# Kernel tuning notes

Measured on AMD Instinct MI355X. Metric: run time of the kernel, lower is better.

The kernel has to match this reference:

```python
import jax, jax.numpy as jnp
import numpy as np

N = 16384   # must equal C**2 so the rel-pos embed broadcasts with x
C = 128     # in_channels
K = 9       # k (min legal for C=128: (2k-1)^2 >= 2C-1)
C_OUT = 256


def setup_inputs() -> dict:
    key = jax.random.key(0)
    k1, k2, k3 = jax.random.split(key, 3)
    x = jax.random.normal(k1, (N, C), dtype=jnp.float32)
    rel_pos_table = jax.random.normal(k2, ((2 * K - 1) ** 2, C), dtype=jnp.float32) * 0.02
    W = jax.random.normal(k3, (2 * C, C_OUT), dtype=jnp.float32) / np.float32(np.sqrt(2 * C))
    b = jnp.zeros((C_OUT,), dtype=jnp.float32)
    return {"x": x, "rel_pos_table": rel_pos_table, "W": W, "b": b}


def _knn_indices(x, k):
    # brute-force kNN (torch_cluster knn_graph, loop=False), dilation=1 -> no edge subsampling
    sq = jnp.sum(x * x, axis=-1)                       # [N]
    d = sq[:, None] + sq[None, :] - 2.0 * (x @ x.T)    # [N, N] squared distances
    d = d.at[jnp.diag_indices(x.shape[0])].set(jnp.inf)  # exclude self-loops
    _, idx = jax.lax.top_k(-d, k)                      # [N, k] nearest neighbors
    return idx


def reference(x, rel_pos_table, W, b):
    n, c = x.shape
    # 1) graph built on RAW x (before rel-pos add), as in the torch forward
    nbr = _knn_indices(x, K)                           # [N, K]
    # 2) learnable relative positional embedding: grid_size = x.shape[1] = C
    ar = jnp.arange(c)
    rel = (ar[:, None] - ar[None, :] + c - 1).reshape(-1)  # [C*C] == [N]
    x = x + rel_pos_table[rel]                         # [N, C]
    # 3) MRConv: max-relative aggregation + concat + 1x1 linear
    x_j = x[nbr]                                       # [N, K, C] neighbor gather
    m = jnp.max(x_j - x[:, None, :], axis=1)           # [N, C] max over neighbors
    return jnp.concatenate([x, m], axis=-1) @ W + b    # [N, C_OUT]
```

## Files before the change

### kernel.cpp

```cpp
#include <hip/hip_runtime.h>

#define NPTS 16384
#define CH 128
#define KNN 9
#define NCAND 12
#define NHALF 4
#define COUT 256
#define RG 16
#define RCAND 3

typedef __attribute__((ext_vector_type(8))) short bf16x8;
typedef __attribute__((ext_vector_type(4))) float f32x4;
typedef __attribute__((address_space(1))) const unsigned gu32;
typedef __attribute__((address_space(3))) unsigned lu32;


__device__ __forceinline__ unsigned bfhi2(float x0, float x1) {
    unsigned u0 = __float_as_uint(x0), u1 = __float_as_uint(x1);
    unsigned r0 = (u0 + 0x7fffu + ((u0 >> 16) & 1u));
    unsigned r1 = (u1 + 0x7fffu + ((u1 >> 16) & 1u));
    return (r0 >> 16) | (r1 & 0xffff0000u);
}

struct TopL {
    float l0,l1,l2,l3,l4,l5,l6,l7,l8,l9,la,lb;
    int   m0,m1,m2,m3,m4,m5,m6,m7,m8,m9,ma,mb;
};
struct Top9 {
    float l0,l1,l2,l3,l4,l5,l6,l7,l8;
    int   m0,m1,m2,m3,m4,m5,m6,m7,m8;
};

__device__ __forceinline__ bool lexlt(float d, int g, float L, int M) {
    return d < L || (d == L && g < M);
}

__device__ __forceinline__ void ins12(TopL& T, float d, int g) {
    if (!lexlt(d, g, T.lb, T.mb)) return;
    bool b0 = lexlt(d,g,T.l0,T.m0);
    bool b1 = lexlt(d,g,T.l1,T.m1);
    bool b2 = lexlt(d,g,T.l2,T.m2);
    bool b3 = lexlt(d,g,T.l3,T.m3);
    bool b4 = lexlt(d,g,T.l4,T.m4);
    bool b5 = lexlt(d,g,T.l5,T.m5);
    bool b6 = lexlt(d,g,T.l6,T.m6);
    bool b7 = lexlt(d,g,T.l7,T.m7);
    bool b8 = lexlt(d,g,T.l8,T.m8);
    bool b9 = lexlt(d,g,T.l9,T.m9);
    bool ba = lexlt(d,g,T.la,T.ma);
    T.lb = ba ? T.la : d;               T.mb = ba ? T.ma : g;
    T.la = b9 ? T.l9 : (ba ? d : T.la); T.ma = b9 ? T.m9 : (ba ? g : T.ma);
    T.l9 = b8 ? T.l8 : (b9 ? d : T.l9); T.m9 = b8 ? T.m8 : (b9 ? g : T.m9);
    T.l8 = b7 ? T.l7 : (b8 ? d : T.l8); T.m8 = b7 ? T.m7 : (b8 ? g : T.m8);
    T.l7 = b6 ? T.l6 : (b7 ? d : T.l7); T.m7 = b6 ? T.m6 : (b7 ? g : T.m7);
    T.l6 = b5 ? T.l5 : (b6 ? d : T.l6); T.m6 = b5 ? T.m5 : (b6 ? g : T.m6);
    T.l5 = b4 ? T.l4 : (b5 ? d : T.l5); T.m5 = b4 ? T.m4 : (b5 ? g : T.m5);
    T.l4 = b3 ? T.l3 : (b4 ? d : T.l4); T.m4 = b3 ? T.m3 : (b4 ? g : T.m4);
    T.l3 = b2 ? T.l2 : (b3 ? d : T.l3); T.m3 = b2 ? T.m2 : (b3 ? g : T.m3);
    T.l2 = b1 ? T.l1 : (b2 ? d : T.l2); T.m2 = b1 ? T.m1 : (b2 ? g : T.m2);
    T.l1 = b0 ? T.l0 : (b1 ? d : T.l1); T.m1 = b0 ? T.m0 : (b1 ? g : T.m1);
    T.l0 = b0 ? d : T.l0;               T.m0 = b0 ? g : T.m0;
}

__device__ __forceinline__ void ins9(Top9& T, float d, int g) {
    if (!lexlt(d, g, T.l8, T.m8)) return;
    bool b0 = lexlt(d,g,T.l0,T.m0);
    bool b1 = lexlt(d,g,T.l1,T.m1);
    bool b2 = lexlt(d,g,T.l2,T.m2);
    bool b3 = lexlt(d,g,T.l3,T.m3);
    bool b4 = lexlt(d,g,T.l4,T.m4);
    bool b5 = lexlt(d,g,T.l5,T.m5);
    bool b6 = lexlt(d,g,T.l6,T.m6);
    bool b7 = lexlt(d,g,T.l7,T.m7);
    T.l8 = b7 ? T.l7 : d;               T.m8 = b7 ? T.m7 : g;
    T.l7 = b6 ? T.l6 : (b7 ? d : T.l7); T.m7 = b6 ? T.m6 : (b7 ? g : T.m7);
    T.l6 = b5 ? T.l5 : (b6 ? d : T.l6); T.m6 = b5 ? T.m5 : (b6 ? g : T.m6);
    T.l5 = b4 ? T.l4 : (b5 ? d : T.l5); T.m5 = b4 ? T.m4 : (b5 ? g : T.m5);
    T.l4 = b3 ? T.l3 : (b4 ? d : T.l4); T.m4 = b3 ? T.m3 : (b4 ? g : T.m4);
    T.l3 = b2 ? T.l2 : (b3 ? d : T.l3); T.m3 = b2 ? T.m2 : (b3 ? g : T.m3);
    T.l2 = b1 ? T.l1 : (b2 ? d : T.l2); T.m2 = b1 ? T.m1 : (b2 ? g : T.m2);
    T.l1 = b0 ? T.l0 : (b1 ? d : T.l1); T.m1 = b0 ? T.m0 : (b1 ? g : T.m1);
    T.l0 = b0 ? d : T.l0;               T.m0 = b0 ? g : T.m0;
}

__device__ __forceinline__ void merge_shfl(TopL& T, int mask) {
    TopL o;
    o.l0=__shfl_xor(T.l0,mask); o.m0=__shfl_xor(T.m0,mask);
    o.l1=__shfl_xor(T.l1,mask); o.m1=__shfl_xor(T.m1,mask);
    o.l2=__shfl_xor(T.l2,mask); o.m2=__shfl_xor(T.m2,mask);
    o.l3=__shfl_xor(T.l3,mask); o.m3=__shfl_xor(T.m3,mask);
    o.l4=__shfl_xor(T.l4,mask); o.m4=__shfl_xor(T.m4,mask);
    o.l5=__shfl_xor(T.l5,mask); o.m5=__shfl_xor(T.m5,mask);
    o.l6=__shfl_xor(T.l6,mask); o.m6=__shfl_xor(T.m6,mask);
    o.l7=__shfl_xor(T.l7,mask); o.m7=__shfl_xor(T.m7,mask);
    o.l8=__shfl_xor(T.l8,mask); o.m8=__shfl_xor(T.m8,mask);
    o.l9=__shfl_xor(T.l9,mask); o.m9=__shfl_xor(T.m9,mask);
    o.la=__shfl_xor(T.la,mask); o.ma=__shfl_xor(T.ma,mask);
    o.lb=__shfl_xor(T.lb,mask); o.mb=__shfl_xor(T.mb,mask);
    ins12(T,o.l0,o.m0); ins12(T,o.l1,o.m1); ins12(T,o.l2,o.m2);
    ins12(T,o.l3,o.m3); ins12(T,o.l4,o.m4); ins12(T,o.l5,o.m5);
    ins12(T,o.l6,o.m6); ins12(T,o.l7,o.m7); ins12(T,o.l8,o.m8);
    ins12(T,o.l9,o.m9); ins12(T,o.la,o.ma); ins12(T,o.lb,o.mb);
}

__device__ __forceinline__ void merge_shfl9(Top9& T, int mask) {
    Top9 o;
    o.l0=__shfl_xor(T.l0,mask); o.m0=__shfl_xor(T.m0,mask);
    o.l1=__shfl_xor(T.l1,mask); o.m1=__shfl_xor(T.m1,mask);
    o.l2=__shfl_xor(T.l2,mask); o.m2=__shfl_xor(T.m2,mask);
    o.l3=__shfl_xor(T.l3,mask); o.m3=__shfl_xor(T.m3,mask);
    o.l4=__shfl_xor(T.l4,mask); o.m4=__shfl_xor(T.m4,mask);
    o.l5=__shfl_xor(T.l5,mask); o.m5=__shfl_xor(T.m5,mask);
    o.l6=__shfl_xor(T.l6,mask); o.m6=__shfl_xor(T.m6,mask);
    o.l7=__shfl_xor(T.l7,mask); o.m7=__shfl_xor(T.m7,mask);
    o.l8=__shfl_xor(T.l8,mask); o.m8=__shfl_xor(T.m8,mask);
    ins9(T,o.l0,o.m0); ins9(T,o.l1,o.m1); ins9(T,o.l2,o.m2);
    ins9(T,o.l3,o.m3); ins9(T,o.l4,o.m4); ins9(T,o.l5,o.m5);
    ins9(T,o.l6,o.m6); ins9(T,o.l7,o.m7); ins9(T,o.l8,o.m8);
}

__global__ __launch_bounds__(256) void sqnp_kernel(const float* __restrict__ x,
                                                   float* __restrict__ sq) {
    const int i = blockIdx.x * 256 + threadIdx.x;
    const float4* row4 = (const float4*)(x + (size_t)i * CH);
    float r[8];
    {
        float4 a = row4[0], b = row4[1];
        r[0] = __fmul_rn(a.x, a.x); r[1] = __fmul_rn(a.y, a.y);
        r[2] = __fmul_rn(a.z, a.z); r[3] = __fmul_rn(a.w, a.w);
        r[4] = __fmul_rn(b.x, b.x); r[5] = __fmul_rn(b.y, b.y);
        r[6] = __fmul_rn(b.z, b.z); r[7] = __fmul_rn(b.w, b.w);
    }
#pragma unroll
    for (int g = 1; g < 16; ++g) {
        float4 a = row4[2 * g], b = row4[2 * g + 1];
        r[0] = __fadd_rn(r[0], __fmul_rn(a.x, a.x));
        r[1] = __fadd_rn(r[1], __fmul_rn(a.y, a.y));
        r[2] = __fadd_rn(r[2], __fmul_rn(a.z, a.z));
        r[3] = __fadd_rn(r[3], __fmul_rn(a.w, a.w));
        r[4] = __fadd_rn(r[4], __fmul_rn(b.x, b.x));
        r[5] = __fadd_rn(r[5], __fmul_rn(b.y, b.y));
        r[6] = __fadd_rn(r[6], __fmul_rn(b.z, b.z));
        r[7] = __fadd_rn(r[7], __fmul_rn(b.w, b.w));
    }
    float t0 = __fadd_rn(__fadd_rn(r[0], r[1]), __fadd_rn(r[2], r[3]));
    float t1 = __fadd_rn(__fadd_rn(r[4], r[5]), __fadd_rn(r[6], r[7]));
    sq[i] = __fadd_rn(t0, t1);
}

__global__ __launch_bounds__(256) void split_kernel(const float* __restrict__ x,
                                                    short* __restrict__ xhi) {
    const int P = blockIdx.x * 256 + threadIdx.x;
    const int r = P >> 4;
    const int s = P & 15;
    const int phys = s ^ (r & 15);
    const float4* src = (const float4*)(x + (size_t)r * CH) + s * 2;
    float4 f0 = src[0], f1 = src[1];
    uint4 h;
    h.x = bfhi2(f0.x, f0.y);
    h.y = bfhi2(f0.z, f0.w);
    h.z = bfhi2(f1.x, f1.y);
    h.w = bfhi2(f1.z, f1.w);
    *(uint4*)&xhi[(size_t)r * 128 + phys * 8] = h;
}

__global__ __launch_bounds__(256, 3) void knn_kernel(const short* __restrict__ xhi,
                                                     const float* __restrict__ sq,
                                                     unsigned short* __restrict__ cand) {
    __shared__ short Bhi[2 * 64 * 128];
    const int t = threadIdx.x;
    const int row0 = blockIdx.x * 64;
    const int half = blockIdx.y;
    const int ctbeg = half * (NPTS / NHALF);
    const int ctend = ctbeg + NPTS / NHALF;

    const int lane = t & 63;
    const int w = t >> 6;
    const int m = lane & 15;
    const int quad = lane >> 4;

#pragma unroll
    for (int it = 0; it < 4; ++it) {
        const int P = t + it * 256;
        __builtin_amdgcn_global_load_lds(
            (gu32*)&xhi[(size_t)ctbeg * 128 + P * 8],
            (lu32*)&Bhi[(it * 256 + w * 64) * 8], 16, 0, 0);
    }
    const short* qrow = xhi + (size_t)(row0 + 16 * w + m) * 128;
    const bf16x8 a0 = *(const bf16x8*)&qrow[((0 * 4 + quad) ^ m) * 8];
    const bf16x8 a1 = *(const bf16x8*)&qrow[((1 * 4 + quad) ^ m) * 8];
    const bf16x8 a2 = *(const bf16x8*)&qrow[((2 * 4 + quad) ^ m) * 8];
    const bf16x8 a3 = *(const bf16x8*)&qrow[((3 * 4 + quad) ^ m) * 8];

    TopL T;
    T.l0=T.l1=T.l2=T.l3=T.l4=T.l5=T.l6=T.l7=T.l8=T.l9=T.la=T.lb = __builtin_inff();
    T.m0=T.m1=T.m2=T.m3=T.m4=T.m5=T.m6=T.m7=T.m8=T.m9=T.ma=T.mb = 0x7fffffff;

    const int qglob = row0 + 16 * w + m;

    float qd0 = __builtin_inff(), qd1 = __builtin_inff();
    int   qg0 = 0x7fffffff,      qg1 = 0x7fffffff;
    int   qn = 0;

    int boff = 0;
    for (int ct = ctbeg; ct < ctend; ct += 64) {
        __syncthreads();

        const short* Bc = Bhi + boff;
        short* Bn = Bhi + (boff ^ (64 * 128));

        const int ctn = ct + 64;
        if (ctn < ctend) {
#pragma unroll
            for (int it = 0; it < 4; ++it) {
                const int P = t + it * 256;
                __builtin_amdgcn_global_load_lds(
                    (gu32*)&xhi[(size_t)ctn * 128 + P * 8],
                    (lu32*)&Bn[(it * 256 + w * 64) * 8], 16, 0, 0);
            }
        }

        f32x4 acc0 = {0.f,0.f,0.f,0.f};
        f32x4 acc1 = {0.f,0.f,0.f,0.f};
        f32x4 acc2 = {0.f,0.f,0.f,0.f};
        f32x4 acc3 = {0.f,0.f,0.f,0.f};

#pragma unroll
        for (int kc = 0; kc < 4; ++kc) {
            const int ks = ((kc * 4 + quad) ^ m) * 8;
            const bf16x8 ah = (kc == 0) ? a0 : (kc == 1) ? a1 : (kc == 2) ? a2 : a3;
            bf16x8 bh0 = *(const bf16x8*)&Bc[(0  + m) * 128 + ks];
            bf16x8 bh1 = *(const bf16x8*)&Bc[(16 + m) * 128 + ks];
            bf16x8 bh2 = *(const bf16x8*)&Bc[(32 + m) * 128 + ks];
            bf16x8 bh3 = *(const bf16x8*)&Bc[(48 + m) * 128 + ks];
            acc0 = __builtin_amdgcn_mfma_f32_16x16x32_bf16(bh0, ah, acc0, 0, 0, 0);
            acc1 = __builtin_amdgcn_mfma_f32_16x16x32_bf16(bh1, ah, acc1, 0, 0, 0);
            acc2 = __builtin_amdgcn_mfma_f32_16x16x32_bf16(bh2, ah, acc2, 0, 0, 0);
            acc3 = __builtin_amdgcn_mfma_f32_16x16x32_bf16(bh3, ah, acc3, 0, 0, 0);
        }

#pragma unroll
        for (int cg = 0; cg < 4; ++cg) {
            const f32x4 ac = (cg == 0) ? acc0 : (cg == 1) ? acc1
                           : (cg == 2) ? acc2 : acc3;
            const float4 s4 = *(const float4*)&sq[ct + cg * 16 + quad * 4];
#pragma unroll
            for (int reg = 0; reg < 4; ++reg) {
                const float sv = (reg == 0) ? s4.x : (reg == 1) ? s4.y
                               : (reg == 2) ? s4.z : s4.w;
                const float d = __builtin_fmaf(-2.f, ac[reg], sv);
                const int cgi = ct + cg * 16 + quad * 4 + reg;
                const bool pass = (d <= T.lb) && (cgi != qglob);
                if (pass) {
                    if (qn >= 2) {
                        ins12(T, d, cgi);
                    } else if (qn == 0) {
                        qd0 = d; qg0 = cgi;
                    } else {
                        qd1 = d; qg1 = cgi;
                    }
                    ++qn;
                }
            }
        }
        if (__any(qn >= 2)) {
            ins12(T, qd0, qg0);
            ins12(T, qd1, qg1);
            qd0 = qd1 = __builtin_inff();
            qg0 = qg1 = 0x7fffffff;
            qn = 0;
        }
        boff ^= 64 * 128;
    }

    ins12(T, qd0, qg0);
    ins12(T, qd1, qg1);
    merge_shfl(T, 16);
    merge_shfl(T, 32);

    if (quad == 0) {
        unsigned short* cp_out = cand + (size_t)qglob * (NHALF * NCAND) + half * NCAND;
        cp_out[0]=(unsigned short)T.m0; cp_out[1]=(unsigned short)T.m1;
        cp_out[2]=(unsigned short)T.m2; cp_out[3]=(unsigned short)T.m3;
        cp_out[4]=(unsigned short)T.m4; cp_out[5]=(unsigned short)T.m5;
        cp_out[6]=(unsigned short)T.m6; cp_out[7]=(unsigned short)T.m7;
        cp_out[8]=(unsigned short)T.m8; cp_out[9]=(unsigned short)T.m9;
        cp_out[10]=(unsigned short)T.ma; cp_out[11]=(unsigned short)T.mb;
    }
}

__global__ __launch_bounds__(256) void refine_np_kernel(const float* __restrict__ x,
                                                        const float* __restrict__ sq,
                                                        const unsigned short* __restrict__ cand,
                                                        unsigned short* __restrict__ nbr) {
    const int gt = blockIdx.x * 256 + threadIdx.x;
    const int i = gt >> 4;
    const int g = gt & (RG - 1);
    const float4* X4 = (const float4*)x;
    const float sqi = sq[i];

    int ci[RCAND];
#pragma unroll
    for (int m = 0; m < RCAND; ++m)
        ci[m] = (int)cand[i * (NHALF * NCAND) + g * RCAND + m];
    float dot[RCAND];
#pragma unroll
    for (int m = 0; m < RCAND; ++m) dot[m] = 0.f;
#pragma unroll 4
    for (int c4 = 0; c4 < 32; ++c4) {
        float4 xv = X4[(size_t)i * 32 + c4];
#pragma unroll
        for (int m = 0; m < RCAND; ++m) {
            float4 nv = X4[(size_t)ci[m] * 32 + c4];
            float a = dot[m];
            a = __builtin_fmaf(xv.x, nv.x, a);
            a = __builtin_fmaf(xv.y, nv.y, a);
            a = __builtin_fmaf(xv.z, nv.z, a);
            a = __builtin_fmaf(xv.w, nv.w, a);
            dot[m] = a;
        }
    }

    Top9 T;
    T.l0=T.l1=T.l2=T.l3=T.l4=T.l5=T.l6=T.l7=T.l8 = __builtin_inff();
    T.m0=T.m1=T.m2=T.m3=T.m4=T.m5=T.m6=T.m7=T.m8 = 0x7fffffff;
#pragma unroll
    for (int m = 0; m < RCAND; ++m) {
        float s = __fadd_rn(sqi, sq[ci[m]]);
        float d = __fsub_rn(s, __fmul_rn(2.0f, dot[m]));
        ins9(T, d, ci[m]);
    }

    merge_shfl9(T, 1);
    merge_shfl9(T, 2);
    merge_shfl9(T, 4);
    merge_shfl9(T, 8);

    if (g == 0) {
        unsigned short* np = nbr + (size_t)i * KNN;
        np[0]=(unsigned short)T.m0; np[1]=(unsigned short)T.m1; np[2]=(unsigned short)T.m2;
        np[3]=(unsigned short)T.m3; np[4]=(unsigned short)T.m4; np[5]=(unsigned short)T.m5;
        np[6]=(unsigned short)T.m6; np[7]=(unsigned short)T.m7; np[8]=(unsigned short)T.m8;
    }
}

__global__ __launch_bounds__(256, 2) void out_kernel(const float* __restrict__ x,
                                                     const float* __restrict__ tab,
                                                     const float* __restrict__ W,
                                                     const float* __restrict__ bias,
                                                     const unsigned short* __restrict__ nbr,
                                                     float* __restrict__ out) {
    __shared__ float cat[32][260];
    const int t = threadIdx.x;
    const int row0 = blockIdx.x * 32;
    {
        const int row = t >> 3;
        const int q = t & 7;
        const int i = row0 + row;
        const int rel_i = (i >> 7) - (i & 127) + 127;
        int nb[KNN], reln[KNN];
#pragma unroll
        for (int j = 0; j < KNN; ++j) {
            nb[j] = (int)nbr[i * KNN + j];
            reln[j] = (nb[j] >> 7) - (nb[j] & 127) + 127;
        }
        const float4* X4 = (const float4*)x;
        const float4* T4 = (const float4*)tab;
#pragma unroll
        for (int cc = 0; cc < 4; ++cc) {
            const int c4 = q * 4 + cc;
            float4 xv = X4[i * 32 + c4];
            float4 tv = T4[rel_i * 32 + c4];
            float4 xi;
            xi.x = xv.x + tv.x; xi.y = xv.y + tv.y; xi.z = xv.z + tv.z; xi.w = xv.w + tv.w;
            const float ninf = -__builtin_inff();
            float4 mx = {ninf, ninf, ninf, ninf};
#pragma unroll
            for (int j = 0; j < KNN; ++j) {
                float4 nv = X4[nb[j] * 32 + c4];
                float4 ntv = T4[reln[j] * 32 + c4];
                mx.x = fmaxf(mx.x, nv.x + ntv.x - xi.x);
                mx.y = fmaxf(mx.y, nv.y + ntv.y - xi.y);
                mx.z = fmaxf(mx.z, nv.z + ntv.z - xi.z);
                mx.w = fmaxf(mx.w, nv.w + ntv.w - xi.w);
            }
            *(float4*)&cat[row][c4 * 4] = xi;
            *(float4*)&cat[row][CH + c4 * 4] = mx;
        }
    }
    __syncthreads();

    float acc[32];
    const float bo = bias[t];
#pragma unroll
    for (int i = 0; i < 32; ++i) acc[i] = bo;
#pragma unroll 2
    for (int c0 = 0; c0 < 2 * CH; c0 += 4) {
        const float w0 = W[(c0 + 0) * COUT + t];
        const float w1 = W[(c0 + 1) * COUT + t];
        const float w2 = W[(c0 + 2) * COUT + t];
        const float w3 = W[(c0 + 3) * COUT + t];
#pragma unroll
        for (int i = 0; i < 32; ++i) {
            const float4 cv = *(const float4*)&cat[i][c0];
            acc[i] = fmaf(cv.x, w0, acc[i]);
            acc[i] = fmaf(cv.y, w1, acc[i]);
            acc[i] = fmaf(cv.z, w2, acc[i]);
            acc[i] = fmaf(cv.w, w3, acc[i]);
        }
    }
#pragma unroll
    for (int i = 0; i < 32; ++i) out[(size_t)(row0 + i) * COUT + t] = acc[i];
}

extern "C" void kernel_launch(void* const* d_in, const int* in_sizes, int n_in,
                              void* d_out, int out_size, void* d_ws, size_t ws_size,
                              hipStream_t stream) {
    (void)in_sizes; (void)n_in; (void)out_size; (void)ws_size;
    const float* x = (const float*)d_in[0];
    const float* tab = (const float*)d_in[1];
    const float* W = (const float*)d_in[2];
    const float* b = (const float*)d_in[3];
    float* out = (float*)d_out;

    char* ws = (char*)d_ws;
    float* sq = (float*)ws;
    unsigned short* nbr = (unsigned short*)(sq + NPTS);

    short* xhi = (short*)d_out;
    unsigned short* cand = (unsigned short*)((char*)d_out + ((size_t)NPTS * CH * 2));

    sqnp_kernel<<<NPTS / 256, 256, 0, stream>>>(x, sq);
    split_kernel<<<NPTS * 16 / 256, 256, 0, stream>>>(x, xhi);
    knn_kernel<<<dim3(NPTS / 64, NHALF), 256, 0, stream>>>(xhi, sq, cand);
    refine_np_kernel<<<NPTS * RG / 256, 256, 0, stream>>>(x, sq, cand, nbr);
    out_kernel<<<NPTS / 32, 256, 0, stream>>>(x, tab, W, b, nbr, out);
}
```

Before: 612.9 us.

## Shrink output GEMM blocks and read a transposed weight matrix with float4 loads

Adds a small kernel that transposes W into a workspace buffer. The output kernel now uses 64-thread blocks that each handle 8 rows, and each thread computes 4 output columns from float4 loads of the transposed weights. The aim is more blocks in flight and vectorised weight loads in the final linear layer. In exchange, every block re-reads the full weight matrix for fewer rows, which cuts weight reuse and raises L2 traffic. Adjacent threads' weight loads are also strided across rows, so they are not coalesced.

Measured after the change: 622.8 us. No clear change (+1.6%).

```diff
diff --git a/kernel.cpp b/kernel.cpp
--- a/kernel.cpp
+++ b/kernel.cpp
@@ -164,6 +164,13 @@
     *(uint4*)&xhi[(size_t)r * 128 + phys * 8] = h;
 }
 
+__global__ __launch_bounds__(256) void wt_kernel(const float* __restrict__ W,
+                                                 float* __restrict__ Wt) {
+    const int c = blockIdx.x;
+    const int k = threadIdx.x;
+    Wt[(size_t)c * (2 * CH) + k] = W[(size_t)k * COUT + c];
+}
+
 __global__ __launch_bounds__(256, 3) void knn_kernel(const short* __restrict__ xhi,
                                                      const float* __restrict__ sq,
                                                      unsigned short* __restrict__ cand) {
@@ -344,15 +351,15 @@
     }
 }
 
-__global__ __launch_bounds__(256, 2) void out_kernel(const float* __restrict__ x,
-                                                     const float* __restrict__ tab,
-                                                     const float* __restrict__ W,
-                                                     const float* __restrict__ bias,
-                                                     const unsigned short* __restrict__ nbr,
-                                                     float* __restrict__ out) {
-    __shared__ float cat[32][260];
+__global__ __launch_bounds__(64) void out_kernel(const float* __restrict__ x,
+                                                 const float* __restrict__ tab,
+                                                 const float* __restrict__ Wt,
+                                                 const float* __restrict__ bias,
+                                                 const unsigned short* __restrict__ nbr,
+                                                 float* __restrict__ out) {
+    __shared__ float cat[8][260];
     const int t = threadIdx.x;
-    const int row0 = blockIdx.x * 32;
+    const int row0 = blockIdx.x * 8;
     {
         const int row = t >> 3;
         const int q = t & 7;
@@ -390,27 +397,50 @@
     }
     __syncthreads();
 
-    float acc[32];
-    const float bo = bias[t];
-#pragma unroll
-    for (int i = 0; i < 32; ++i) acc[i] = bo;
+    float acc[8][4];
+#pragma unroll
+    for (int c = 0; c < 4; ++c) {
+        const float bo = bias[t + 64 * c];
+#pragma unroll
+        for (int i = 0; i < 8; ++i) acc[i][c] = bo;
+    }
+
+    const float4* WT4 = (const float4*)Wt;
 #pragma unroll 2
-    for (int c0 = 0; c0 < 2 * CH; c0 += 4) {
-        const float w0 = W[(c0 + 0) * COUT + t];
-        const float w1 = W[(c0 + 1) * COUT + t];
-        const float w2 = W[(c0 + 2) * COUT + t];
-        const float w3 = W[(c0 + 3) * COUT + t];
-#pragma unroll
-        for (int i = 0; i < 32; ++i) {
-            const float4 cv = *(const float4*)&cat[i][c0];
-            acc[i] = fmaf(cv.x, w0, acc[i]);
-            acc[i] = fmaf(cv.y, w1, acc[i]);
-            acc[i] = fmaf(cv.z, w2, acc[i]);
-            acc[i] = fmaf(cv.w, w3, acc[i]);
-        }
-    }
-#pragma unroll
-    for (int i = 0; i < 32; ++i) out[(size_t)(row0 + i) * COUT + t] = acc[i];
+    for (int c04 = 0; c04 < 64; ++c04) {
+        float4 wv0 = WT4[(size_t)(t +   0) * 64 + c04];
+        float4 wv1 = WT4[(size_t)(t +  64) * 64 + c04];
+        float4 wv2 = WT4[(size_t)(t + 128) * 64 + c04];
+        float4 wv3 = WT4[(size_t)(t + 192) * 64 + c04];
+#pragma unroll
+        for (int i = 0; i < 8; ++i) {
+            const float4 cv = *(const float4*)&cat[i][c04 * 4];
+            acc[i][0] = fmaf(cv.x, wv0.x, acc[i][0]);
+            acc[i][0] = fmaf(cv.y, wv0.y, acc[i][0]);
+            acc[i][0] = fmaf(cv.z, wv0.z, acc[i][0]);
+            acc[i][0] = fmaf(cv.w, wv0.w, acc[i][0]);
+            acc[i][1] = fmaf(cv.x, wv1.x, acc[i][1]);
+            acc[i][1] = fmaf(cv.y, wv1.y, acc[i][1]);
+            acc[i][1] = fmaf(cv.z, wv1.z, acc[i][1]);
+            acc[i][1] = fmaf(cv.w, wv1.w, acc[i][1]);
+            acc[i][2] = fmaf(cv.x, wv2.x, acc[i][2]);
+            acc[i][2] = fmaf(cv.y, wv2.y, acc[i][2]);
+            acc[i][2] = fmaf(cv.z, wv2.z, acc[i][2]);
+            acc[i][2] = fmaf(cv.w, wv2.w, acc[i][2]);
+            acc[i][3] = fmaf(cv.x, wv3.x, acc[i][3]);
+            acc[i][3] = fmaf(cv.y, wv3.y, acc[i][3]);
+            acc[i][3] = fmaf(cv.z, wv3.z, acc[i][3]);
+            acc[i][3] = fmaf(cv.w, wv3.w, acc[i][3]);
+        }
+    }
+
+#pragma unroll
+    for (int i = 0; i < 8; ++i) {
+#pragma unroll
+        for (int c = 0; c < 4; ++c) {
+            out[(size_t)(row0 + i) * COUT + t + 64 * c] = acc[i][c];
+        }
+    }
 }
 
 extern "C" void kernel_launch(void* const* d_in, const int* in_sizes, int n_in,
@@ -426,13 +456,15 @@
     char* ws = (char*)d_ws;
     float* sq = (float*)ws;
     unsigned short* nbr = (unsigned short*)(sq + NPTS);
+    float* Wt = (float*)(ws + 64 * 1024 + 288 * 1024);
 
     short* xhi = (short*)d_out;
     unsigned short* cand = (unsigned short*)((char*)d_out + ((size_t)NPTS * CH * 2));
 
     sqnp_kernel<<<NPTS / 256, 256, 0, stream>>>(x, sq);
     split_kernel<<<NPTS * 16 / 256, 256, 0, stream>>>(x, xhi);
+    wt_kernel<<<COUT, 2 * CH, 0, stream>>>(W, Wt);
     knn_kernel<<<dim3(NPTS / 64, NHALF), 256, 0, stream>>>(xhi, sq, cand);
     refine_np_kernel<<<NPTS * RG / 256, 256, 0, stream>>>(x, sq, cand, nbr);
-    out_kernel<<<NPTS / 32, 256, 0, stream>>>(x, tab, W, b, nbr, out);
-}
+    out_kernel<<<NPTS / 8, 64, 0, stream>>>(x, tab, Wt, b, nbr, out);
+}
```
